# Optimization experiments

Hardware: AMD Instinct MI355X
Metric: run time of the kernel (lower is better)

Reference implementation:

```python
import jax, jax.numpy as jnp
import numpy as np


def setup_inputs() -> dict:
    key = jax.random.key(0)
    k1, k2 = jax.random.split(key)
    x = jax.random.normal(k1, (8, 8192, 512), dtype=jnp.float32)
    codebook = jax.random.normal(k2, (1024, 512), dtype=jnp.float32)
    return {"x": x, "codebook": codebook}


def reference(x, codebook):
    # torch.cdist -> Euclidean distance; argmin is invariant under sqrt, so
    x2 = jnp.sum(x * x, axis=-1, keepdims=True)          # [B, N, 1]
    c2 = jnp.sum(codebook * codebook, axis=-1)           # [K]
    xc = jnp.einsum('bnd,kd->bnk', x, codebook)          # [B, N, K]
    d2 = x2 - 2.0 * xc + c2                              # [B, N, K]
    idx = jnp.argmin(d2, axis=-1)                        # [B, N]
    return codebook[idx]                                 # [B, N, dim]
```

## Files before the change

kernel.cpp:

```cpp
#include <hip/hip_runtime.h>
#include <cstdio>


typedef float f32x4 __attribute__((ext_vector_type(4)));
typedef _Float16 half8 __attribute__((ext_vector_type(8)));

#define KDIM 512
#define NCODES 1024
#define NQ 65536
#define TAU_S 0.05f

#define WS_XH    0ull
#define WS_CBH   67108864ull
#define WS_C2H   68157440ull
#define WS_C2D   68161536ull
#define WS_CAND1 68169728ull
#define WS_CBT   WS_CAND1
#define WS_CAND2 69218304ull
#define WS_CANDC 70266880ull
#define WS_IDX   71315456ull
#define WS_LIST  71577600ull
#define WS_CTR   71839744ull
#define WS_NEED  (WS_CTR + 4ull)

__device__ __forceinline__ unsigned short f2h(float f) {
  _Float16 h = (_Float16)f;
  return __builtin_bit_cast(unsigned short, h);
}

__device__ __forceinline__ void async16(const void* g, void* l) {
  __builtin_amdgcn_global_load_lds(
      (const __attribute__((address_space(1))) void*)g,
      (__attribute__((address_space(3))) void*)l, 16, 0, 0);
}

__global__ __launch_bounds__(256) void vq_prep(const float* __restrict__ cb,
                                               unsigned short* __restrict__ cbh,
                                               float* __restrict__ c2h,
                                               double* __restrict__ c2d) {
  int lane = threadIdx.x & 63;
  int row = blockIdx.x * 4 + (threadIdx.x >> 6);
  const float4* src = (const float4*)(cb + (size_t)row * KDIM);
  float4 u = src[lane * 2], v = src[lane * 2 + 1];
  double p = (double)u.x * u.x + (double)u.y * u.y + (double)u.z * u.z + (double)u.w * u.w +
             (double)v.x * v.x + (double)v.y * v.y + (double)v.z * v.z + (double)v.w * v.w;
#pragma unroll
  for (int m = 1; m < 64; m <<= 1) p += __shfl_xor(p, m);
  if (lane == 0) { c2h[row] = (float)(0.5 * p); c2d[row] = 0.5 * p; }
  unsigned r0 = f2h(u.x) | ((unsigned)f2h(u.y) << 16);
  unsigned r1 = f2h(u.z) | ((unsigned)f2h(u.w) << 16);
  unsigned r2 = f2h(v.x) | ((unsigned)f2h(v.y) << 16);
  unsigned r3 = f2h(v.z) | ((unsigned)f2h(v.w) << 16);
  *(int4*)(cbh + (size_t)row * KDIM + lane * 8) = make_int4((int)r0, (int)r1, (int)r2, (int)r3);
}

__global__ __launch_bounds__(256) void vq_convx(const float4* __restrict__ x4,
                                                int4* __restrict__ xh4) {
  size_t t = (size_t)blockIdx.x * 256 + threadIdx.x;
  float4 u = x4[t * 2], v = x4[t * 2 + 1];
  unsigned r0 = f2h(u.x) | ((unsigned)f2h(u.y) << 16);
  unsigned r1 = f2h(u.z) | ((unsigned)f2h(u.w) << 16);
  unsigned r2 = f2h(v.x) | ((unsigned)f2h(v.y) << 16);
  unsigned r3 = f2h(v.z) | ((unsigned)f2h(v.w) << 16);
  xh4[t] = make_int4((int)r0, (int)r1, (int)r2, (int)r3);
}

__global__ __launch_bounds__(1024, 4) void vq_main(const unsigned short* __restrict__ xh,
                                                   const unsigned short* __restrict__ cbh,
                                                   const float* __restrict__ c2h,
                                                   float* __restrict__ cand1,
                                                   float* __restrict__ cand2,
                                                   int* __restrict__ candc) {
  __shared__ char pool[65536];
  unsigned short* As0 = (unsigned short*)pool;
  unsigned short* Bs0 = (unsigned short*)(pool + 32768);
  float* red1 = (float*)pool;
  float* red2 = (float*)(pool + 4096);
  int*   redc = (int*)(pool + 8192);

  const int tid = threadIdx.x;
  const int lane = tid & 63, wv = tid >> 6;
  const int mw = wv & 3, nw = wv >> 2;
  const int c = lane & 15, q = lane >> 4;
  const int mb = blockIdx.x >> 2, nb = blockIdx.x & 3;

  const int r0 = tid >> 2, g0 = tid & 3;
  const int s0 = (r0 >> 1) & 3;
  const size_t xrow0 = (size_t)(mb * 256 + r0) * KDIM + ((g0 ^ s0) * 8);
  const size_t crow0 = (size_t)(nb * 256 + r0) * KDIM + ((g0 ^ s0) * 8);

  f32x4 acc[4][4];
#pragma unroll
  for (int i = 0; i < 4; ++i)
#pragma unroll
    for (int j = 0; j < 4; ++j) acc[i][j] = (f32x4){0.f, 0.f, 0.f, 0.f};

  async16(xh + xrow0,  &As0[tid * 8]);
  async16(cbh + crow0, &Bs0[tid * 8]);

  for (int ko = 0; ko < 16; ++ko) {
    const int cur = ko & 1;
    __syncthreads();
    if (ko + 1 < 16) {
      const int k0 = (ko + 1) * 32;
      async16(xh + xrow0 + k0,  &As0[(1 - cur) * 8192 + tid * 8]);
      async16(cbh + crow0 + k0, &Bs0[(1 - cur) * 8192 + tid * 8]);
    }
    const unsigned short* A = &As0[cur * 8192];
    const unsigned short* B = &Bs0[cur * 8192];
    half8 a[4], b[4];
#pragma unroll
    for (int i = 0; i < 4; ++i) {
      int mr = mw * 64 + i * 16 + c;
      a[i] = *(const half8*)&A[mr * 32 + ((q ^ ((mr >> 1) & 3)) * 8)];
    }
#pragma unroll
    for (int j = 0; j < 4; ++j) {
      int nr = nw * 64 + j * 16 + c;
      b[j] = *(const half8*)&B[nr * 32 + ((q ^ ((nr >> 1) & 3)) * 8)];
    }
#pragma unroll
    for (int i = 0; i < 4; ++i)
#pragma unroll
      for (int j = 0; j < 4; ++j)
        acc[i][j] = __builtin_amdgcn_mfma_f32_16x16x32_f16(a[i], b[j], acc[i][j], 0, 0, 0);
  }

  float mn1[4][4], mn2[4][4];
  int mcol[4][4];
#pragma unroll
  for (int i = 0; i < 4; ++i)
#pragma unroll
    for (int r = 0; r < 4; ++r) { mn1[i][r] = 1e30f; mn2[i][r] = 1e30f; mcol[i][r] = 0; }
#pragma unroll
  for (int j = 0; j < 4; ++j) {
    int colb = nb * 256 + nw * 64 + j * 16 + c;
    float c2v = c2h[colb];
#pragma unroll
    for (int i = 0; i < 4; ++i)
#pragma unroll
      for (int r = 0; r < 4; ++r) {
        float sv = c2v - acc[i][j][r];
        float hi = fmaxf(sv, mn1[i][r]);
        mn2[i][r] = fminf(mn2[i][r], hi);
        bool lt = sv < mn1[i][r];
        mn1[i][r] = lt ? sv : mn1[i][r];
        mcol[i][r] = lt ? colb : mcol[i][r];
      }
  }
#pragma unroll
  for (int m = 1; m < 16; m <<= 1) {
#pragma unroll
    for (int i = 0; i < 4; ++i)
#pragma unroll
      for (int r = 0; r < 4; ++r) {
        float o1 = __shfl_xor(mn1[i][r], m);
        float o2 = __shfl_xor(mn2[i][r], m);
        int   oc = __shfl_xor(mcol[i][r], m);
        float hi = fmaxf(o1, mn1[i][r]);
        mn2[i][r] = fminf(fminf(mn2[i][r], o2), hi);
        bool lt = o1 < mn1[i][r];
        mn1[i][r] = lt ? o1 : mn1[i][r];
        mcol[i][r] = lt ? oc : mcol[i][r];
      }
  }
  if (c == 0) {
#pragma unroll
    for (int i = 0; i < 4; ++i)
#pragma unroll
      for (int r = 0; r < 4; ++r) {
        int rb = mw * 64 + i * 16 + q * 4 + r;
        red1[rb * 4 + nw] = mn1[i][r];
        red2[rb * 4 + nw] = mn2[i][r];
        redc[rb * 4 + nw] = mcol[i][r];
      }
  }
  __syncthreads();
  if (tid < 256) {
    float b1 = red1[tid * 4], b2 = red2[tid * 4];
    int bc = redc[tid * 4];
#pragma unroll
    for (int w = 1; w < 4; ++w) {
      float o1 = red1[tid * 4 + w], o2 = red2[tid * 4 + w];
      int oc = redc[tid * 4 + w];
      float hi = fmaxf(o1, b1);
      b2 = fminf(fminf(b2, o2), hi);
      if (o1 < b1) { b1 = o1; bc = oc; }
    }
    size_t qg = (size_t)(mb * 256 + tid) * 4 + nb;
    cand1[qg] = b1; cand2[qg] = b2; candc[qg] = bc;
  }
}

__global__ __launch_bounds__(256) void vq_reduce(const float4* __restrict__ c1,
                                                 const float4* __restrict__ c2,
                                                 const int4* __restrict__ cc,
                                                 int* __restrict__ idx,
                                                 int* __restrict__ list,
                                                 int* __restrict__ counter) {
  int qg = blockIdx.x * 256 + threadIdx.x;
  float4 a1 = c1[qg];
  float4 a2 = c2[qg];
  int4 ai = cc[qg];
  float m1[4] = {a1.x, a1.y, a1.z, a1.w};
  float m2[4] = {a2.x, a2.y, a2.z, a2.w};
  int mc[4] = {ai.x, ai.y, ai.z, ai.w};
  float g1 = m1[0], g2 = m2[0];
  int gc = mc[0];
#pragma unroll
  for (int k = 1; k < 4; ++k) {
    float hi = fmaxf(m1[k], g1);
    g2 = fminf(fminf(g2, m2[k]), hi);
    if (m1[k] < g1) { g1 = m1[k]; gc = mc[k]; }
  }
  idx[qg] = gc;
  if (g2 - g1 < TAU_S) { int p = atomicAdd(counter, 1); list[p] = qg; }
}

__global__ __launch_bounds__(256) void vq_trans(const float4* __restrict__ cb4,
                                                float4* __restrict__ cbT4) {
  __shared__ float t[64][65];
  const int bc = blockIdx.x >> 3, bk = blockIdx.x & 7;
  const int c0 = bc * 64, k0 = bk * 64;
  const int r = threadIdx.x >> 4, q4 = threadIdx.x & 15;
#pragma unroll
  for (int p = 0; p < 4; ++p) {
    int row = p * 16 + r;
    float4 v = cb4[(size_t)(c0 + row) * 128 + (k0 >> 2) + q4];
    t[row][q4 * 4 + 0] = v.x; t[row][q4 * 4 + 1] = v.y;
    t[row][q4 * 4 + 2] = v.z; t[row][q4 * 4 + 3] = v.w;
  }
  __syncthreads();
#pragma unroll
  for (int p = 0; p < 4; ++p) {
    int kk = p * 16 + r;
    float4 v = make_float4(t[q4 * 4 + 0][kk], t[q4 * 4 + 1][kk],
                           t[q4 * 4 + 2][kk], t[q4 * 4 + 3][kk]);
    cbT4[(size_t)(k0 + kk) * 256 + (c0 >> 2) + q4] = v;
  }
}

__global__ __launch_bounds__(256) void vq_refine(const float* __restrict__ x,
                                                 const float4* __restrict__ cbT4,
                                                 const double* __restrict__ c2d,
                                                 const int* __restrict__ list,
                                                 const int* __restrict__ counter,
                                                 int* __restrict__ idx) {
  __shared__ float xs[512];
  __shared__ double rv[4];
  __shared__ int rc[4];
  const int cnt = counter[0];
  const int tid = threadIdx.x, lane = tid & 63, wv = tid >> 6;
  for (int qi = blockIdx.x; qi < cnt; qi += gridDim.x) {
    const int query = list[qi];
    __syncthreads();
    xs[tid] = x[(size_t)query * KDIM + tid];
    xs[tid + 256] = x[(size_t)query * KDIM + tid + 256];
    __syncthreads();
    double a0 = 0, a1 = 0, a2 = 0, a3 = 0;
    const float4* xs4 = (const float4*)xs;
#pragma unroll 4
    for (int k4 = 0; k4 < 128; ++k4) {
      float4 xv = xs4[k4];
      float4 c0 = cbT4[(k4 * 4 + 0) * 256 + tid];
      float4 c1 = cbT4[(k4 * 4 + 1) * 256 + tid];
      float4 c2v = cbT4[(k4 * 4 + 2) * 256 + tid];
      float4 c3 = cbT4[(k4 * 4 + 3) * 256 + tid];
      a0 = fma((double)xv.x, (double)c0.x, a0);
      a1 = fma((double)xv.x, (double)c0.y, a1);
      a2 = fma((double)xv.x, (double)c0.z, a2);
      a3 = fma((double)xv.x, (double)c0.w, a3);
      a0 = fma((double)xv.y, (double)c1.x, a0);
      a1 = fma((double)xv.y, (double)c1.y, a1);
      a2 = fma((double)xv.y, (double)c1.z, a2);
      a3 = fma((double)xv.y, (double)c1.w, a3);
      a0 = fma((double)xv.z, (double)c2v.x, a0);
      a1 = fma((double)xv.z, (double)c2v.y, a1);
      a2 = fma((double)xv.z, (double)c2v.z, a2);
      a3 = fma((double)xv.z, (double)c2v.w, a3);
      a0 = fma((double)xv.w, (double)c3.x, a0);
      a1 = fma((double)xv.w, (double)c3.y, a1);
      a2 = fma((double)xv.w, (double)c3.z, a2);
      a3 = fma((double)xv.w, (double)c3.w, a3);
    }
    double best = c2d[tid * 4] - a0;
    int bc = tid * 4;
    double s1 = c2d[tid * 4 + 1] - a1;
    if (s1 < best) { best = s1; bc = tid * 4 + 1; }
    double s2 = c2d[tid * 4 + 2] - a2;
    if (s2 < best) { best = s2; bc = tid * 4 + 2; }
    double s3 = c2d[tid * 4 + 3] - a3;
    if (s3 < best) { best = s3; bc = tid * 4 + 3; }
#pragma unroll
    for (int m = 1; m < 64; m <<= 1) {
      double o = __shfl_xor(best, m);
      int oc = __shfl_xor(bc, m);
      if (o < best) { best = o; bc = oc; }
    }
    if (lane == 0) { rv[wv] = best; rc[wv] = bc; }
    __syncthreads();
    if (tid == 0) {
      double b = rv[0]; int bci = rc[0];
#pragma unroll
      for (int w = 1; w < 4; ++w)
        if (rv[w] < b) { b = rv[w]; bci = rc[w]; }
      idx[query] = bci;
    }
    __syncthreads();
  }
}

__global__ __launch_bounds__(256) void vq_gather(const float* __restrict__ cb,
                                                 const int* __restrict__ idx,
                                                 float* __restrict__ out) {
  size_t i = (size_t)blockIdx.x * 256 + threadIdx.x;
  int qg = (int)(i >> 7), d = (int)(i & 127);
  ((float4*)out)[i] = ((const float4*)cb)[(size_t)idx[qg] * 128 + d];
}

extern "C" void kernel_launch(void* const* d_in, const int* in_sizes, int n_in,
                              void* d_out, int out_size, void* d_ws, size_t ws_size,
                              hipStream_t stream) {
  const float* x = (const float*)d_in[0];
  const float* cb = (const float*)d_in[1];
  float* out = (float*)d_out;
  char* ws = (char*)d_ws;
  if (ws_size < WS_NEED) {
    fprintf(stderr, "vq: ws_size %zu too small (need %llu)\n", ws_size,
            (unsigned long long)WS_NEED);
    return;
  }
  unsigned short* xh = (unsigned short*)(ws + WS_XH);
  unsigned short* cbh = (unsigned short*)(ws + WS_CBH);
  float* c2h = (float*)(ws + WS_C2H);
  double* c2d = (double*)(ws + WS_C2D);
  float* cand1 = (float*)(ws + WS_CAND1);
  float* cand2 = (float*)(ws + WS_CAND2);
  int* candc = (int*)(ws + WS_CANDC);
  float* cbT = (float*)(ws + WS_CBT);
  int* idx = (int*)(ws + WS_IDX);
  int* list = (int*)(ws + WS_LIST);
  int* counter = (int*)(ws + WS_CTR);

  hipMemsetAsync(counter, 0, 4, stream);
  vq_prep<<<256, 256, 0, stream>>>(cb, cbh, c2h, c2d);
  vq_convx<<<16384, 256, 0, stream>>>((const float4*)x, (int4*)xh);
  vq_main<<<1024, 1024, 0, stream>>>(xh, cbh, c2h, cand1, cand2, candc);
  vq_reduce<<<256, 256, 0, stream>>>((const float4*)cand1, (const float4*)cand2,
                                     (const int4*)candc, idx, list, counter);
  vq_trans<<<128, 256, 0, stream>>>((const float4*)cb, (float4*)cbT);
  vq_refine<<<2048, 256, 0, stream>>>(x, (const float4*)cbT, c2d, list, counter, idx);
  vq_gather<<<32768, 256, 0, stream>>>(cb, idx, out);
}
```

Baseline: 419.6 us.

## Restructure fp16 distance GEMM into 8-wave 256x256 tile with K=64 ping-pong pipeline

Rewrites the main distance GEMM to use 512 threads (8 waves), each wave computing a 128x64 output tile. The K loop now steps by 64 with double-buffered async LDS staging split into halves interleaved between MFMA clusters. It adds explicit barriers, waitcnt and setprio scheduling, plus a new 8-column XOR swizzle. The aim is more reuse per wave and overlap of global loads with MFMA issue. In exchange it needs more accumulator registers and tight manual synchronisation.

```diff
diff --git a/kernel.cpp b/kernel.cpp
--- a/kernel.cpp
+++ b/kernel.cpp
@@ -65,115 +65,176 @@
   xh4[t] = make_int4((int)r0, (int)r1, (int)r2, (int)r3);
 }
 
-__global__ __launch_bounds__(1024, 4) void vq_main(const unsigned short* __restrict__ xh,
-                                                   const unsigned short* __restrict__ cbh,
-                                                   const float* __restrict__ c2h,
-                                                   float* __restrict__ cand1,
-                                                   float* __restrict__ cand2,
-                                                   int* __restrict__ candc) {
-  __shared__ char pool[65536];
-  unsigned short* As0 = (unsigned short*)pool;
-  unsigned short* Bs0 = (unsigned short*)(pool + 32768);
-  float* red1 = (float*)pool;
-  float* red2 = (float*)(pool + 4096);
-  int*   redc = (int*)(pool + 8192);
+#define PBAR __builtin_amdgcn_s_barrier()
+#define SB0  __builtin_amdgcn_sched_barrier(0)
+#define LGKM0 do { asm volatile("s_waitcnt lgkmcnt(0)" ::: "memory"); SB0; } while (0)
+
+__global__ __launch_bounds__(512, 2) void vq_main(const unsigned short* __restrict__ xh,
+                                                  const unsigned short* __restrict__ cbh,
+                                                  const float* __restrict__ c2h,
+                                                  float* __restrict__ cand1,
+                                                  float* __restrict__ cand2,
+                                                  int* __restrict__ candc) {
+  __shared__ unsigned short lds[65536];
+  unsigned short* As = lds;
+  unsigned short* Bs = lds + 32768;
+  float* red1 = (float*)lds;
+  float* red2 = (float*)(lds + 2048);
+  int*   redc = (int*)(lds + 4096);
 
   const int tid = threadIdx.x;
   const int lane = tid & 63, wv = tid >> 6;
-  const int mw = wv & 3, nw = wv >> 2;
+  const int mw = wv >> 2, nw = wv & 3;
   const int c = lane & 15, q = lane >> 4;
   const int mb = blockIdx.x >> 2, nb = blockIdx.x & 3;
 
-  const int r0 = tid >> 2, g0 = tid & 3;
-  const int s0 = (r0 >> 1) & 3;
-  const size_t xrow0 = (size_t)(mb * 256 + r0) * KDIM + ((g0 ^ s0) * 8);
-  const size_t crow0 = (size_t)(nb * 256 + r0) * KDIM + ((g0 ^ s0) * 8);
-
-  f32x4 acc[4][4];
-#pragma unroll
-  for (int i = 0; i < 4; ++i)
+  const int srow = tid >> 3;
+  const int scol = ((tid & 7) ^ (srow & 7)) * 8;
+  const unsigned short* ax[2][2];
+  const unsigned short* bx[2][2];
+#pragma unroll
+  for (int h = 0; h < 2; ++h)
+#pragma unroll
+    for (int l = 0; l < 2; ++l) {
+      int row = h * 128 + l * 64 + srow;
+      ax[h][l] = xh  + (size_t)(mb * 256 + row) * KDIM + scol;
+      bx[h][l] = cbh + (size_t)(nb * 256 + row) * KDIM + scol;
+    }
+
+#define STAGE_A(tt, h) do { \
+    int _bo = ((tt) & 1) * 16384 + (h) * 8192 + tid * 8; \
+    async16(ax[h][0] + (tt) * 64, &As[_bo]); \
+    async16(ax[h][1] + (tt) * 64, &As[_bo + 4096]); } while (0)
+#define STAGE_B(tt, h) do { \
+    int _bo = ((tt) & 1) * 16384 + (h) * 8192 + tid * 8; \
+    async16(bx[h][0] + (tt) * 64, &Bs[_bo]); \
+    async16(bx[h][1] + (tt) * 64, &Bs[_bo + 4096]); } while (0)
+
+  const int swz = (c & 7) * 8;
+  const int acol0 = (q * 8) ^ swz;
+  const int acol1 = acol0 ^ 32;
+  const int aro = (mw * 128 + c) * 64;
+  const int bro = (nw * 64 + c) * 64;
+#define RDA(buf, i, ks) (*(const half8*)&As[(buf) * 16384 + aro + (i) * 1024 + ((ks) ? acol1 : acol0)])
+#define RDB(buf, j, ks) (*(const half8*)&Bs[(buf) * 16384 + bro + (j) * 1024 + ((ks) ? acol1 : acol0)])
+
+  f32x4 acc[8][4];
+#pragma unroll
+  for (int i = 0; i < 8; ++i)
 #pragma unroll
     for (int j = 0; j < 4; ++j) acc[i][j] = (f32x4){0.f, 0.f, 0.f, 0.f};
-
-  async16(xh + xrow0,  &As0[tid * 8]);
-  async16(cbh + crow0, &Bs0[tid * 8]);
-
-  for (int ko = 0; ko < 16; ++ko) {
-    const int cur = ko & 1;
-    __syncthreads();
-    if (ko + 1 < 16) {
-      const int k0 = (ko + 1) * 32;
-      async16(xh + xrow0 + k0,  &As0[(1 - cur) * 8192 + tid * 8]);
-      async16(cbh + crow0 + k0, &Bs0[(1 - cur) * 8192 + tid * 8]);
-    }
-    const unsigned short* A = &As0[cur * 8192];
-    const unsigned short* B = &Bs0[cur * 8192];
-    half8 a[4], b[4];
-#pragma unroll
-    for (int i = 0; i < 4; ++i) {
-      int mr = mw * 64 + i * 16 + c;
-      a[i] = *(const half8*)&A[mr * 32 + ((q ^ ((mr >> 1) & 3)) * 8)];
-    }
+  half8 a[4][2], b[4][2];
+
+  STAGE_A(0, 0); STAGE_A(0, 1); STAGE_B(0, 0); STAGE_B(0, 1);
+  STAGE_A(1, 0); STAGE_A(1, 1); STAGE_B(1, 0); STAGE_B(1, 1);
+  asm volatile("s_waitcnt vmcnt(8)" ::: "memory");
+  PBAR;
+
+#pragma unroll
+  for (int t = 0; t < 8; ++t) {
+    const int cb = t & 1;
+#pragma unroll
+    for (int ii = 0; ii < 4; ++ii) { a[ii][0] = RDA(cb, ii, 0); a[ii][1] = RDA(cb, ii, 1); }
+#pragma unroll
+    for (int j = 0; j < 2; ++j) { b[j][0] = RDB(cb, j, 0); b[j][1] = RDB(cb, j, 1); }
+    if (t >= 1 && t < 7) { STAGE_A(t + 1, 0); STAGE_B(t + 1, 0); }
+    PBAR; LGKM0;
+    __builtin_amdgcn_s_setprio(1);
+#pragma unroll
+    for (int ii = 0; ii < 4; ++ii)
+#pragma unroll
+      for (int j = 0; j < 2; ++j)
+#pragma unroll
+        for (int ks = 0; ks < 2; ++ks)
+          acc[ii][j] = __builtin_amdgcn_mfma_f32_16x16x32_f16(a[ii][ks], b[j][ks], acc[ii][j], 0, 0, 0);
+    __builtin_amdgcn_s_setprio(0); SB0; PBAR;
+#pragma unroll
+    for (int j = 2; j < 4; ++j) { b[j][0] = RDB(cb, j, 0); b[j][1] = RDB(cb, j, 1); }
+    if (t >= 1 && t < 7) { STAGE_A(t + 1, 1); STAGE_B(t + 1, 1); }
+    PBAR; LGKM0;
+    __builtin_amdgcn_s_setprio(1);
+#pragma unroll
+    for (int ii = 0; ii < 4; ++ii)
+#pragma unroll
+      for (int j = 2; j < 4; ++j)
+#pragma unroll
+        for (int ks = 0; ks < 2; ++ks)
+          acc[ii][j] = __builtin_amdgcn_mfma_f32_16x16x32_f16(a[ii][ks], b[j][ks], acc[ii][j], 0, 0, 0);
+    __builtin_amdgcn_s_setprio(0); SB0; PBAR;
+#pragma unroll
+    for (int ii = 0; ii < 4; ++ii) { a[ii][0] = RDA(cb, 4 + ii, 0); a[ii][1] = RDA(cb, 4 + ii, 1); }
+    PBAR; LGKM0;
+    __builtin_amdgcn_s_setprio(1);
+#pragma unroll
+    for (int ii = 0; ii < 4; ++ii)
+#pragma unroll
+      for (int j = 0; j < 2; ++j)
+#pragma unroll
+        for (int ks = 0; ks < 2; ++ks)
+          acc[4 + ii][j] = __builtin_amdgcn_mfma_f32_16x16x32_f16(a[ii][ks], b[j][ks], acc[4 + ii][j], 0, 0, 0);
+    __builtin_amdgcn_s_setprio(0); SB0; PBAR;
+    __builtin_amdgcn_s_setprio(1);
+#pragma unroll
+    for (int ii = 0; ii < 4; ++ii)
+#pragma unroll
+      for (int j = 2; j < 4; ++j)
+#pragma unroll
+        for (int ks = 0; ks < 2; ++ks)
+          acc[4 + ii][j] = __builtin_amdgcn_mfma_f32_16x16x32_f16(a[ii][ks], b[j][ks], acc[4 + ii][j], 0, 0, 0);
+    __builtin_amdgcn_s_setprio(0); SB0;
+    asm volatile("s_waitcnt vmcnt(0)" ::: "memory");
+    PBAR;
+  }
+#undef STAGE_A
+#undef STAGE_B
+#undef RDA
+#undef RDB
+
+  float c2v[4];
+#pragma unroll
+  for (int j = 0; j < 4; ++j) c2v[j] = c2h[nb * 256 + nw * 64 + j * 16 + c];
+#pragma unroll
+  for (int i = 0; i < 8; ++i) {
+    float m1[4], m2[4];
+    int mc[4];
+#pragma unroll
+    for (int r = 0; r < 4; ++r) { m1[r] = 1e30f; m2[r] = 1e30f; mc[r] = 0; }
 #pragma unroll
     for (int j = 0; j < 4; ++j) {
-      int nr = nw * 64 + j * 16 + c;
-      b[j] = *(const half8*)&B[nr * 32 + ((q ^ ((nr >> 1) & 3)) * 8)];
-    }
-#pragma unroll
-    for (int i = 0; i < 4; ++i)
-#pragma unroll
-      for (int j = 0; j < 4; ++j)
-        acc[i][j] = __builtin_amdgcn_mfma_f32_16x16x32_f16(a[i], b[j], acc[i][j], 0, 0, 0);
-  }
-
-  float mn1[4][4], mn2[4][4];
-  int mcol[4][4];
-#pragma unroll
-  for (int i = 0; i < 4; ++i)
-#pragma unroll
-    for (int r = 0; r < 4; ++r) { mn1[i][r] = 1e30f; mn2[i][r] = 1e30f; mcol[i][r] = 0; }
-#pragma unroll
-  for (int j = 0; j < 4; ++j) {
-    int colb = nb * 256 + nw * 64 + j * 16 + c;
-    float c2v = c2h[colb];
-#pragma unroll
-    for (int i = 0; i < 4; ++i)
+      int colb = nb * 256 + nw * 64 + j * 16 + c;
 #pragma unroll
       for (int r = 0; r < 4; ++r) {
-        float sv = c2v - acc[i][j][r];
-        float hi = fmaxf(sv, mn1[i][r]);
-        mn2[i][r] = fminf(mn2[i][r], hi);
-        bool lt = sv < mn1[i][r];
-        mn1[i][r] = lt ? sv : mn1[i][r];
-        mcol[i][r] = lt ? colb : mcol[i][r];
+        float sv = c2v[j] - acc[i][j][r];
+        float hi = fmaxf(sv, m1[r]);
+        m2[r] = fminf(m2[r], hi);
+        bool lt = sv < m1[r];
+        m1[r] = lt ? sv : m1[r];
+        mc[r] = lt ? colb : mc[r];
       }
-  }
-#pragma unroll
-  for (int m = 1; m < 16; m <<= 1) {
-#pragma unroll
-    for (int i = 0; i < 4; ++i)
+    }
+#pragma unroll
+    for (int m = 1; m < 16; m <<= 1) {
 #pragma unroll
       for (int r = 0; r < 4; ++r) {
-        float o1 = __shfl_xor(mn1[i][r], m);
-        float o2 = __shfl_xor(mn2[i][r], m);
-        int   oc = __shfl_xor(mcol[i][r], m);
-        float hi = fmaxf(o1, mn1[i][r]);
-        mn2[i][r] = fminf(fminf(mn2[i][r], o2), hi);
-        bool lt = o1 < mn1[i][r];
-        mn1[i][r] = lt ? o1 : mn1[i][r];
-        mcol[i][r] = lt ? oc : mcol[i][r];
+        float o1 = __shfl_xor(m1[r], m);
+        float o2 = __shfl_xor(m2[r], m);
+        int   oc = __shfl_xor(mc[r], m);
+        float hi = fmaxf(o1, m1[r]);
+        m2[r] = fminf(fminf(m2[r], o2), hi);
+        bool lt = o1 < m1[r];
+        m1[r] = lt ? o1 : m1[r];
+        mc[r] = lt ? oc : mc[r];
       }
-  }
-  if (c == 0) {
-#pragma unroll
-    for (int i = 0; i < 4; ++i)
+    }
+    if (c == 0) {
 #pragma unroll
       for (int r = 0; r < 4; ++r) {
-        int rb = mw * 64 + i * 16 + q * 4 + r;
-        red1[rb * 4 + nw] = mn1[i][r];
-        red2[rb * 4 + nw] = mn2[i][r];
-        redc[rb * 4 + nw] = mcol[i][r];
+        int rb = mw * 128 + i * 16 + q * 4 + r;
+        red1[rb * 4 + nw] = m1[r];
+        red2[rb * 4 + nw] = m2[r];
+        redc[rb * 4 + nw] = mc[r];
       }
+    }
   }
   __syncthreads();
   if (tid < 256) {
@@ -345,7 +406,7 @@
   hipMemsetAsync(counter, 0, 4, stream);
   vq_prep<<<256, 256, 0, stream>>>(cb, cbh, c2h, c2d);
   vq_convx<<<16384, 256, 0, stream>>>((const float4*)x, (int4*)xh);
-  vq_main<<<1024, 1024, 0, stream>>>(xh, cbh, c2h, cand1, cand2, candc);
+  vq_main<<<1024, 512, 0, stream>>>(xh, cbh, c2h, cand1, cand2, candc);
   vq_reduce<<<256, 256, 0, stream>>>((const float4*)cand1, (const float4*)cand2,
                                      (const int4*)candc, idx, list, counter);
   vq_trans<<<128, 256, 0, stream>>>((const float4*)cb, (float4*)cbT);
```

New measurement: 414.6 us. About the same (-1.2%).

## Fuse x fp16 conversion and argmin reduction into main kernel; batch refine queries

Applied to the files above, without the earlier changes.

The main kernel now reads fp32 x directly, converts to fp16 in registers, and keeps each wave's 32 query rows resident while streaming the entire codebook through double-buffered LDS. This removes the separate convx and reduce kernels and the candidate workspace round trips. The refine kernel now processes 8 flagged queries per block so each codebook load is reused across several queries. In exchange the main grid drops to 256 blocks of 512 threads with a large 132KB LDS footprint and heavy register use, which may lower occupancy.

```diff
diff --git a/kernel.cpp b/kernel.cpp
--- a/kernel.cpp
+++ b/kernel.cpp
@@ -10,17 +10,13 @@
 #define NQ 65536
 #define TAU_S 0.05f
 
-#define WS_XH    0ull
-#define WS_CBH   67108864ull
-#define WS_C2H   68157440ull
-#define WS_C2D   68161536ull
-#define WS_CAND1 68169728ull
-#define WS_CBT   WS_CAND1
-#define WS_CAND2 69218304ull
-#define WS_CANDC 70266880ull
-#define WS_IDX   71315456ull
-#define WS_LIST  71577600ull
-#define WS_CTR   71839744ull
+#define WS_CBH   0ull
+#define WS_C2H   1048576ull
+#define WS_C2D   1052672ull
+#define WS_CBT   1060864ull
+#define WS_IDX   3158016ull
+#define WS_LIST  3420160ull
+#define WS_CTR   3682304ull
 #define WS_NEED  (WS_CTR + 4ull)
 
 __device__ __forceinline__ unsigned short f2h(float f) {
@@ -54,167 +50,154 @@
   *(int4*)(cbh + (size_t)row * KDIM + lane * 8) = make_int4((int)r0, (int)r1, (int)r2, (int)r3);
 }
 
-__global__ __launch_bounds__(256) void vq_convx(const float4* __restrict__ x4,
-                                                int4* __restrict__ xh4) {
-  size_t t = (size_t)blockIdx.x * 256 + threadIdx.x;
-  float4 u = x4[t * 2], v = x4[t * 2 + 1];
-  unsigned r0 = f2h(u.x) | ((unsigned)f2h(u.y) << 16);
-  unsigned r1 = f2h(u.z) | ((unsigned)f2h(u.w) << 16);
-  unsigned r2 = f2h(v.x) | ((unsigned)f2h(v.y) << 16);
-  unsigned r3 = f2h(v.z) | ((unsigned)f2h(v.w) << 16);
-  xh4[t] = make_int4((int)r0, (int)r1, (int)r2, (int)r3);
-}
-
-__global__ __launch_bounds__(1024, 4) void vq_main(const unsigned short* __restrict__ xh,
-                                                   const unsigned short* __restrict__ cbh,
-                                                   const float* __restrict__ c2h,
-                                                   float* __restrict__ cand1,
-                                                   float* __restrict__ cand2,
-                                                   int* __restrict__ candc) {
-  __shared__ char pool[65536];
-  unsigned short* As0 = (unsigned short*)pool;
-  unsigned short* Bs0 = (unsigned short*)(pool + 32768);
-  float* red1 = (float*)pool;
-  float* red2 = (float*)(pool + 4096);
-  int*   redc = (int*)(pool + 8192);
+__global__ __launch_bounds__(512, 2) void vq_main(const float* __restrict__ x,
+                                                  const unsigned short* __restrict__ cbh,
+                                                  const float* __restrict__ c2h,
+                                                  int* __restrict__ idx,
+                                                  int* __restrict__ list,
+                                                  int* __restrict__ counter) {
+  __shared__ __align__(16) char pool[135168];
+  float* c2s = (float*)(pool + 131072);
 
   const int tid = threadIdx.x;
   const int lane = tid & 63, wv = tid >> 6;
-  const int mw = wv & 3, nw = wv >> 2;
   const int c = lane & 15, q = lane >> 4;
-  const int mb = blockIdx.x >> 2, nb = blockIdx.x & 3;
-
-  const int r0 = tid >> 2, g0 = tid & 3;
-  const int s0 = (r0 >> 1) & 3;
-  const size_t xrow0 = (size_t)(mb * 256 + r0) * KDIM + ((g0 ^ s0) * 8);
-  const size_t crow0 = (size_t)(nb * 256 + r0) * KDIM + ((g0 ^ s0) * 8);
-
-  f32x4 acc[4][4];
-#pragma unroll
-  for (int i = 0; i < 4; ++i)
-#pragma unroll
-    for (int j = 0; j < 4; ++j) acc[i][j] = (f32x4){0.f, 0.f, 0.f, 0.f};
-
-  async16(xh + xrow0,  &As0[tid * 8]);
-  async16(cbh + crow0, &Bs0[tid * 8]);
-
-  for (int ko = 0; ko < 16; ++ko) {
-    const int cur = ko & 1;
-    __syncthreads();
-    if (ko + 1 < 16) {
-      const int k0 = (ko + 1) * 32;
-      async16(xh + xrow0 + k0,  &As0[(1 - cur) * 8192 + tid * 8]);
-      async16(cbh + crow0 + k0, &Bs0[(1 - cur) * 8192 + tid * 8]);
-    }
-    const unsigned short* A = &As0[cur * 8192];
-    const unsigned short* B = &Bs0[cur * 8192];
-    half8 a[4], b[4];
-#pragma unroll
-    for (int i = 0; i < 4; ++i) {
-      int mr = mw * 64 + i * 16 + c;
-      a[i] = *(const half8*)&A[mr * 32 + ((q ^ ((mr >> 1) & 3)) * 8)];
-    }
-#pragma unroll
-    for (int j = 0; j < 4; ++j) {
-      int nr = nw * 64 + j * 16 + c;
-      b[j] = *(const half8*)&B[nr * 32 + ((q ^ ((nr >> 1) & 3)) * 8)];
-    }
-#pragma unroll
-    for (int i = 0; i < 4; ++i)
-#pragma unroll
-      for (int j = 0; j < 4; ++j)
-        acc[i][j] = __builtin_amdgcn_mfma_f32_16x16x32_f16(a[i], b[j], acc[i][j], 0, 0, 0);
-  }
-
-  float mn1[4][4], mn2[4][4];
-  int mcol[4][4];
-#pragma unroll
-  for (int i = 0; i < 4; ++i)
-#pragma unroll
-    for (int r = 0; r < 4; ++r) { mn1[i][r] = 1e30f; mn2[i][r] = 1e30f; mcol[i][r] = 0; }
-#pragma unroll
-  for (int j = 0; j < 4; ++j) {
-    int colb = nb * 256 + nw * 64 + j * 16 + c;
-    float c2v = c2h[colb];
-#pragma unroll
-    for (int i = 0; i < 4; ++i)
+  const int qbase = blockIdx.x * 256 + wv * 32;
+
+#define STAGE(cc) do {                                                        \
+    const unsigned short* _s = cbh + (size_t)(cc) * 32768 + wv * 4096;        \
+    char* _d = pool + (((cc) & 1) * 65536) + wv * 8192 + lane * 16;           \
+    _Pragma("unroll")                                                         \
+    for (int s = 0; s < 8; ++s)                                               \
+      async16(_s + s * 512 + ((lane ^ s) * 8), _d + s * 1024); } while (0)
+
+  if (wv < 4) async16(c2h + (wv * 64 + lane) * 4, pool + 131072 + wv * 1024 + lane * 16);
+  STAGE(0);
+
+  half8 a[2][16];
+  {
+    const float* xr0 = x + (size_t)(qbase + c) * KDIM + q * 8;
+    const float* xr1 = xr0 + (size_t)16 * KDIM;
+    float4 t0[8], t1[8];
+#pragma unroll
+    for (int gj = 0; gj < 4; ++gj) {
+      const float* p = xr0 + gj * 32;
+      t0[gj * 2] = *(const float4*)p;
+      t0[gj * 2 + 1] = *(const float4*)(p + 4);
+    }
+#pragma unroll
+    for (int g = 0; g < 8; ++g) {
+      if (g + 1 < 8) {
+#pragma unroll
+        for (int gj = 0; gj < 4; ++gj) {
+          const int fi = (g + 1) * 4 + gj;
+          const int rf = fi >> 4, kf = fi & 15;
+          const float* p = (rf ? xr1 : xr0) + kf * 32;
+          if ((g + 1) & 1) {
+            t1[gj * 2] = *(const float4*)p; t1[gj * 2 + 1] = *(const float4*)(p + 4);
+          } else {
+            t0[gj * 2] = *(const float4*)p; t0[gj * 2 + 1] = *(const float4*)(p + 4);
+          }
+        }
+      }
+#pragma unroll
+      for (int gj = 0; gj < 4; ++gj) {
+        const int fi = g * 4 + gj;
+        const int rf = fi >> 4, kf = fi & 15;
+        float4 lo, hi;
+        if (g & 1) { lo = t1[gj * 2]; hi = t1[gj * 2 + 1]; }
+        else       { lo = t0[gj * 2]; hi = t0[gj * 2 + 1]; }
+        half8 h;
+        h[0] = (_Float16)lo.x; h[1] = (_Float16)lo.y;
+        h[2] = (_Float16)lo.z; h[3] = (_Float16)lo.w;
+        h[4] = (_Float16)hi.x; h[5] = (_Float16)hi.y;
+        h[6] = (_Float16)hi.z; h[7] = (_Float16)hi.w;
+        a[rf][kf] = h;
+      }
+      __builtin_amdgcn_sched_barrier(0);
+    }
+  }
+
+  float m1[2][4], m2[2][4];
+  int mcx[2][4];
+#pragma unroll
+  for (int i = 0; i < 2; ++i)
+#pragma unroll
+    for (int r = 0; r < 4; ++r) { m1[i][r] = 1e30f; m2[i][r] = 1e30f; mcx[i][r] = 0; }
+
+  const int crow = c * 512;
+  const int m3 = c & 7;
+
+#pragma unroll 1
+  for (int ch = 0; ch < 16; ++ch) {
+    __syncthreads();
+    if (ch + 1 < 16) STAGE(ch + 1);
+
+    const unsigned short* B = (const unsigned short*)(pool + ((ch & 1) * 65536));
+    f32x4 acc[2][4];
+#pragma unroll
+    for (int i = 0; i < 2; ++i)
+#pragma unroll
+      for (int j = 0; j < 4; ++j) acc[i][j] = (f32x4){0.f, 0.f, 0.f, 0.f};
+
+#pragma unroll
+    for (int kf = 0; kf < 16; ++kf) {
+      half8 b[4];
+      const int gg = (kf * 4 + q) ^ m3;
+#pragma unroll
+      for (int cf = 0; cf < 4; ++cf)
+        b[cf] = *(const half8*)&B[cf * 8192 + crow + gg * 8];
+#pragma unroll
+      for (int i = 0; i < 2; ++i)
+#pragma unroll
+        for (int cf = 0; cf < 4; ++cf)
+          acc[i][cf] = __builtin_amdgcn_mfma_f32_16x16x32_f16(a[i][kf], b[cf], acc[i][cf], 0, 0, 0);
+    }
+#pragma unroll
+    for (int cf = 0; cf < 4; ++cf) {
+      const int col = ch * 64 + cf * 16 + c;
+      const float c2v = c2s[col];
+#pragma unroll
+      for (int i = 0; i < 2; ++i)
+#pragma unroll
+        for (int r = 0; r < 4; ++r) {
+          float sv = c2v - acc[i][cf][r];
+          float hi = fmaxf(sv, m1[i][r]);
+          m2[i][r] = fminf(m2[i][r], hi);
+          bool lt = sv < m1[i][r];
+          m1[i][r] = lt ? sv : m1[i][r];
+          mcx[i][r] = lt ? col : mcx[i][r];
+        }
+    }
+  }
+#undef STAGE
+
+#pragma unroll
+  for (int m = 1; m < 16; m <<= 1) {
+#pragma unroll
+    for (int i = 0; i < 2; ++i)
 #pragma unroll
       for (int r = 0; r < 4; ++r) {
-        float sv = c2v - acc[i][j][r];
-        float hi = fmaxf(sv, mn1[i][r]);
-        mn2[i][r] = fminf(mn2[i][r], hi);
-        bool lt = sv < mn1[i][r];
-        mn1[i][r] = lt ? sv : mn1[i][r];
-        mcol[i][r] = lt ? colb : mcol[i][r];
-      }
-  }
-#pragma unroll
-  for (int m = 1; m < 16; m <<= 1) {
-#pragma unroll
-    for (int i = 0; i < 4; ++i)
+        float o1 = __shfl_xor(m1[i][r], m);
+        float o2 = __shfl_xor(m2[i][r], m);
+        int   oc = __shfl_xor(mcx[i][r], m);
+        float hi = fmaxf(o1, m1[i][r]);
+        m2[i][r] = fminf(fminf(m2[i][r], o2), hi);
+        bool lt = o1 < m1[i][r];
+        m1[i][r] = lt ? o1 : m1[i][r];
+        mcx[i][r] = lt ? oc : mcx[i][r];
+      }
+  }
+  if (c == 0) {
+#pragma unroll
+    for (int i = 0; i < 2; ++i)
 #pragma unroll
       for (int r = 0; r < 4; ++r) {
-        float o1 = __shfl_xor(mn1[i][r], m);
-        float o2 = __shfl_xor(mn2[i][r], m);
-        int   oc = __shfl_xor(mcol[i][r], m);
-        float hi = fmaxf(o1, mn1[i][r]);
-        mn2[i][r] = fminf(fminf(mn2[i][r], o2), hi);
-        bool lt = o1 < mn1[i][r];
-        mn1[i][r] = lt ? o1 : mn1[i][r];
-        mcol[i][r] = lt ? oc : mcol[i][r];
-      }
-  }
-  if (c == 0) {
-#pragma unroll
-    for (int i = 0; i < 4; ++i)
-#pragma unroll
-      for (int r = 0; r < 4; ++r) {
-        int rb = mw * 64 + i * 16 + q * 4 + r;
-        red1[rb * 4 + nw] = mn1[i][r];
-        red2[rb * 4 + nw] = mn2[i][r];
-        redc[rb * 4 + nw] = mcol[i][r];
-      }
-  }
-  __syncthreads();
-  if (tid < 256) {
-    float b1 = red1[tid * 4], b2 = red2[tid * 4];
-    int bc = redc[tid * 4];
-#pragma unroll
-    for (int w = 1; w < 4; ++w) {
-      float o1 = red1[tid * 4 + w], o2 = red2[tid * 4 + w];
-      int oc = redc[tid * 4 + w];
-      float hi = fmaxf(o1, b1);
-      b2 = fminf(fminf(b2, o2), hi);
-      if (o1 < b1) { b1 = o1; bc = oc; }
-    }
-    size_t qg = (size_t)(mb * 256 + tid) * 4 + nb;
-    cand1[qg] = b1; cand2[qg] = b2; candc[qg] = bc;
-  }
-}
-
-__global__ __launch_bounds__(256) void vq_reduce(const float4* __restrict__ c1,
-                                                 const float4* __restrict__ c2,
-                                                 const int4* __restrict__ cc,
-                                                 int* __restrict__ idx,
-                                                 int* __restrict__ list,
-                                                 int* __restrict__ counter) {
-  int qg = blockIdx.x * 256 + threadIdx.x;
-  float4 a1 = c1[qg];
-  float4 a2 = c2[qg];
-  int4 ai = cc[qg];
-  float m1[4] = {a1.x, a1.y, a1.z, a1.w};
-  float m2[4] = {a2.x, a2.y, a2.z, a2.w};
-  int mc[4] = {ai.x, ai.y, ai.z, ai.w};
-  float g1 = m1[0], g2 = m2[0];
-  int gc = mc[0];
-#pragma unroll
-  for (int k = 1; k < 4; ++k) {
-    float hi = fmaxf(m1[k], g1);
-    g2 = fminf(fminf(g2, m2[k]), hi);
-    if (m1[k] < g1) { g1 = m1[k]; gc = mc[k]; }
-  }
-  idx[qg] = gc;
-  if (g2 - g1 < TAU_S) { int p = atomicAdd(counter, 1); list[p] = qg; }
+        int query = qbase + i * 16 + q * 4 + r;
+        idx[query] = mcx[i][r];
+        if (m2[i][r] - m1[i][r] < TAU_S) { int p = atomicAdd(counter, 1); list[p] = query; }
+      }
+  }
 }
 
 __global__ __launch_bounds__(256) void vq_trans(const float4* __restrict__ cb4,
@@ -246,67 +229,83 @@
                                                  const int* __restrict__ list,
                                                  const int* __restrict__ counter,
                                                  int* __restrict__ idx) {
-  __shared__ float xs[512];
-  __shared__ double rv[4];
-  __shared__ int rc[4];
+  __shared__ __align__(16) float xs[8][512];
+  __shared__ int qlist[8];
+  __shared__ double rv[8][4];
+  __shared__ int rc[8][4];
   const int cnt = counter[0];
   const int tid = threadIdx.x, lane = tid & 63, wv = tid >> 6;
-  for (int qi = blockIdx.x; qi < cnt; qi += gridDim.x) {
-    const int query = list[qi];
-    __syncthreads();
-    xs[tid] = x[(size_t)query * KDIM + tid];
-    xs[tid + 256] = x[(size_t)query * KDIM + tid + 256];
-    __syncthreads();
-    double a0 = 0, a1 = 0, a2 = 0, a3 = 0;
-    const float4* xs4 = (const float4*)xs;
-#pragma unroll 4
+  for (int base = blockIdx.x * 8; base < cnt; base += gridDim.x * 8) {
+    const int nq = min(8, cnt - base);
+    __syncthreads();
+    if (tid < 8) qlist[tid] = list[base + ((tid < nq) ? tid : 0)];
+    __syncthreads();
+#pragma unroll
+    for (int k = 0; k < 4; ++k) {
+      int e = tid + 256 * k;
+      int qi = e >> 7, d4 = e & 127;
+      ((float4*)xs)[e] = ((const float4*)(x + (size_t)qlist[qi] * KDIM))[d4];
+    }
+    __syncthreads();
+    double a0[8], a1[8], a2[8], a3[8];
+#pragma unroll
+    for (int qi = 0; qi < 8; ++qi) { a0[qi] = 0; a1[qi] = 0; a2[qi] = 0; a3[qi] = 0; }
+#pragma unroll 2
     for (int k4 = 0; k4 < 128; ++k4) {
-      float4 xv = xs4[k4];
       float4 c0 = cbT4[(k4 * 4 + 0) * 256 + tid];
       float4 c1 = cbT4[(k4 * 4 + 1) * 256 + tid];
       float4 c2v = cbT4[(k4 * 4 + 2) * 256 + tid];
       float4 c3 = cbT4[(k4 * 4 + 3) * 256 + tid];
-      a0 = fma((double)xv.x, (double)c0.x, a0);
-      a1 = fma((double)xv.x, (double)c0.y, a1);
-      a2 = fma((double)xv.x, (double)c0.z, a2);
-      a3 = fma((double)xv.x, (double)c0.w, a3);
-      a0 = fma((double)xv.y, (double)c1.x, a0);
-      a1 = fma((double)xv.y, (double)c1.y, a1);
-      a2 = fma((double)xv.y, (double)c1.z, a2);
-      a3 = fma((double)xv.y, (double)c1.w, a3);
-      a0 = fma((double)xv.z, (double)c2v.x, a0);
-      a1 = fma((double)xv.z, (double)c2v.y, a1);
-      a2 = fma((double)xv.z, (double)c2v.z, a2);
-      a3 = fma((double)xv.z, (double)c2v.w, a3);
-      a0 = fma((double)xv.w, (double)c3.x, a0);
-      a1 = fma((double)xv.w, (double)c3.y, a1);
-      a2 = fma((double)xv.w, (double)c3.z, a2);
-      a3 = fma((double)xv.w, (double)c3.w, a3);
-    }
-    double best = c2d[tid * 4] - a0;
-    int bc = tid * 4;
-    double s1 = c2d[tid * 4 + 1] - a1;
-    if (s1 < best) { best = s1; bc = tid * 4 + 1; }
-    double s2 = c2d[tid * 4 + 2] - a2;
-    if (s2 < best) { best = s2; bc = tid * 4 + 2; }
-    double s3 = c2d[tid * 4 + 3] - a3;
-    if (s3 < best) { best = s3; bc = tid * 4 + 3; }
-#pragma unroll
-    for (int m = 1; m < 64; m <<= 1) {
-      double o = __shfl_xor(best, m);
-      int oc = __shfl_xor(bc, m);
-      if (o < best) { best = o; bc = oc; }
-    }
-    if (lane == 0) { rv[wv] = best; rc[wv] = bc; }
-    __syncthreads();
-    if (tid == 0) {
-      double b = rv[0]; int bci = rc[0];
+#pragma unroll
+      for (int qi = 0; qi < 8; ++qi) {
+        float4 xv = *(const float4*)&xs[qi][k4 * 4];
+        a0[qi] = fma((double)xv.x, (double)c0.x, a0[qi]);
+        a1[qi] = fma((double)xv.x, (double)c0.y, a1[qi]);
+        a2[qi] = fma((double)xv.x, (double)c0.z, a2[qi]);
+        a3[qi] = fma((double)xv.x, (double)c0.w, a3[qi]);
+        a0[qi] = fma((double)xv.y, (double)c1.x, a0[qi]);
+        a1[qi] = fma((double)xv.y, (double)c1.y, a1[qi]);
+        a2[qi] = fma((double)xv.y, (double)c1.z, a2[qi]);
+        a3[qi] = fma((double)xv.y, (double)c1.w, a3[qi]);
+        a0[qi] = fma((double)xv.z, (double)c2v.x, a0[qi]);
+        a1[qi] = fma((double)xv.z, (double)c2v.y, a1[qi]);
+        a2[qi] = fma((double)xv.z, (double)c2v.z, a2[qi]);
+        a3[qi] = fma((double)xv.z, (double)c2v.w, a3[qi]);
+        a0[qi] = fma((double)xv.w, (double)c3.x, a0[qi]);
+        a1[qi] = fma((double)xv.w, (double)c3.y, a1[qi]);
+        a2[qi] = fma((double)xv.w, (double)c3.z, a2[qi]);
+        a3[qi] = fma((double)xv.w, (double)c3.w, a3[qi]);
+      }
+    }
+    const double c2l0 = c2d[tid * 4], c2l1 = c2d[tid * 4 + 1];
+    const double c2l2 = c2d[tid * 4 + 2], c2l3 = c2d[tid * 4 + 3];
+#pragma unroll
+    for (int qi = 0; qi < 8; ++qi) {
+      double best = c2l0 - a0[qi];
+      int bc = tid * 4;
+      double s1 = c2l1 - a1[qi];
+      if (s1 < best) { best = s1; bc = tid * 4 + 1; }
+      double s2 = c2l2 - a2[qi];
+      if (s2 < best) { best = s2; bc = tid * 4 + 2; }
+      double s3 = c2l3 - a3[qi];
+      if (s3 < best) { best = s3; bc = tid * 4 + 3; }
+#pragma unroll
+      for (int m = 1; m < 64; m <<= 1) {
+        double o = __shfl_xor(best, m);
+        int oc = __shfl_xor(bc, m);
+        if (o < best) { best = o; bc = oc; }
+      }
+      if (lane == 0) { rv[qi][wv] = best; rc[qi][wv] = bc; }
+    }
+    __syncthreads();
+    if (tid < nq) {
+      double b = rv[tid][0];
+      int bci = rc[tid][0];
 #pragma unroll
       for (int w = 1; w < 4; ++w)
-        if (rv[w] < b) { b = rv[w]; bci = rc[w]; }
-      idx[query] = bci;
-    }
-    __syncthreads();
+        if (rv[tid][w] < b) { b = rv[tid][w]; bci = rc[tid][w]; }
+      idx[qlist[tid]] = bci;
+    }
   }
 }
 
@@ -330,13 +329,9 @@
             (unsigned long long)WS_NEED);
     return;
   }
-  unsigned short* xh = (unsigned short*)(ws + WS_XH);
   unsigned short* cbh = (unsigned short*)(ws + WS_CBH);
   float* c2h = (float*)(ws + WS_C2H);
   double* c2d = (double*)(ws + WS_C2D);
-  float* cand1 = (float*)(ws + WS_CAND1);
-  float* cand2 = (float*)(ws + WS_CAND2);
-  int* candc = (int*)(ws + WS_CANDC);
   float* cbT = (float*)(ws + WS_CBT);
   int* idx = (int*)(ws + WS_IDX);
   int* list = (int*)(ws + WS_LIST);
@@ -344,11 +339,8 @@
 
   hipMemsetAsync(counter, 0, 4, stream);
   vq_prep<<<256, 256, 0, stream>>>(cb, cbh, c2h, c2d);
-  vq_convx<<<16384, 256, 0, stream>>>((const float4*)x, (int4*)xh);
-  vq_main<<<1024, 1024, 0, stream>>>(xh, cbh, c2h, cand1, cand2, candc);
-  vq_reduce<<<256, 256, 0, stream>>>((const float4*)cand1, (const float4*)cand2,
-                                     (const int4*)candc, idx, list, counter);
   vq_trans<<<128, 256, 0, stream>>>((const float4*)cb, (float4*)cbT);
+  vq_main<<<256, 512, 0, stream>>>(x, cbh, c2h, idx, list, counter);
   vq_refine<<<2048, 256, 0, stream>>>(x, (const float4*)cbT, c2d, list, counter, idx);
   vq_gather<<<32768, 256, 0, stream>>>(cb, idx, out);
 }
```

New measurement: 418.6 us. About the same (-0.2%).
